# Kernel tuning notes

Hardware: AMD Instinct MI355X
Metric: run time of the kernel (lower is better)

Reference implementation:

```python
import jax, jax.numpy as jnp
import numpy as np

# Keras GRUCell math (reset_after=True default), weights SHARED across all
# num_layers stacked cells (faithful to `[self.rnn_cell for _ in range(L)]`).
NUM_LAYERS = 3
HID = 128


def setup_inputs() -> dict:
    key = jax.random.key(0)
    ks = jax.random.split(key, 4)
    B, T, D, H = 64, 2048, HID, HID
    s = 1.0 / np.sqrt(H)
    return {
        "X": jax.random.uniform(ks[0], (B, T, D), dtype=jnp.float32),
        "kernel": jax.random.normal(ks[1], (D, 3 * H), dtype=jnp.float32) * s,
        "rec_kernel": jax.random.normal(ks[2], (H, 3 * H), dtype=jnp.float32) * s,
        "bias_in": jnp.zeros((3 * H,), dtype=jnp.float32),
        "bias_rec": jnp.zeros((3 * H,), dtype=jnp.float32),
        "W_out": jax.random.normal(ks[3], (H, H), dtype=jnp.float32) * s,
        "b_out": jnp.zeros((H,), dtype=jnp.float32),
    }


def _gru_layer(seq_tbd, kernel, rec_kernel, bias_in, bias_rec):
    # seq_tbd: [T, B, D] -> [T, B, H]
    H = rec_kernel.shape[0]
    B = seq_tbd.shape[1]

    def step(h, x):
        gx = x @ kernel + bias_in            # [B, 3H]
        gh = h @ rec_kernel + bias_rec       # [B, 3H]
        xz, xr, xh = jnp.split(gx, 3, axis=-1)
        hz, hr, hh = jnp.split(gh, 3, axis=-1)
        z = jax.nn.sigmoid(xz + hz)          # update gate
        r = jax.nn.sigmoid(xr + hr)          # reset gate
        cand = jnp.tanh(xh + r * hh)         # candidate state
        h_new = z * h + (1.0 - z) * cand
        return h_new, h_new

    h0 = jnp.zeros((B, H), dtype=seq_tbd.dtype)
    _, out = jax.lax.scan(step, h0, seq_tbd)
    return out


def reference(X, kernel, rec_kernel, bias_in, bias_rec, W_out, b_out):
    seq = jnp.transpose(X, (1, 0, 2))  # [T, B, D]
    for _ in range(NUM_LAYERS):
        seq = _gru_layer(seq, kernel, rec_kernel, bias_in, bias_rec)
    out = jnp.transpose(seq, (1, 0, 2))  # [B, T, H]
    return jax.nn.sigmoid(out @ W_out + b_out)
```

## Files before the change

kernel.cpp:

```cpp
#include <hip/hip_runtime.h>
#include <stdint.h>

#define TSEQ 2048
#define NB   64
#define HD   128
#define G3   384
#define W_RING 512
#define SLOT_U32 (16*128)
#define RING_BYTES ((size_t)12 * W_RING * SLOT_U32 * 4)
#define FLAGS_OFF RING_BYTES

typedef __bf16 bf16_t;
typedef __bf16 bf16x8 __attribute__((ext_vector_type(8)));
typedef float  f32x4  __attribute__((ext_vector_type(4)));
typedef unsigned long long ull;

union B8 { uint4 u; bf16x8 v; unsigned a4[4]; };
union HU { bf16_t h; unsigned short u; };
static_assert(sizeof(B8) == 16, "B8 must be 16B");

__device__ __forceinline__ float fast_sigmoid(float x) {
    float e = __builtin_amdgcn_exp2f(-1.44269504f * x);
    return __builtin_amdgcn_rcpf(1.0f + e);
}
__device__ __forceinline__ float fast_tanh(float x) {
    x = fminf(9.0f, fmaxf(-9.0f, x));
    float e = __builtin_amdgcn_exp2f(2.88539008f * x);
    return 1.0f - 2.0f * __builtin_amdgcn_rcpf(1.0f + e);
}

#define MFMA16(A_, B_, C_) (C_) = __builtin_amdgcn_mfma_f32_16x16x32_bf16((A_), (B_), (C_), 0, 0, 0)

__device__ __forceinline__ ull ld_agent_u64(const ull* p) {
    return __hip_atomic_load(p, __ATOMIC_RELAXED, __HIP_MEMORY_SCOPE_AGENT);
}
__device__ __forceinline__ void st_agent_u32(unsigned* p, unsigned v) {
    __hip_atomic_store(p, v, __ATOMIC_RELAXED, __HIP_MEMORY_SCOPE_AGENT);
}
__device__ __forceinline__ unsigned ld_flag_acq(const unsigned* p) {
    return __hip_atomic_load(p, __ATOMIC_ACQUIRE, __HIP_MEMORY_SCOPE_AGENT);
}
__device__ __forceinline__ void st_flag_rel(unsigned* p, unsigned v) {
    __hip_atomic_store(p, v, __ATOMIC_RELEASE, __HIP_MEMORY_SCOPE_AGENT);
}
__device__ __forceinline__ unsigned spin_until(const unsigned* f, unsigned need,
                                               unsigned cur, bool& dead) {
    if (cur >= need) return cur;
    if (dead) return need;
    int g = 0;
    do {
        unsigned s = ld_flag_acq(f);
        if (s >= need) return s;
        __builtin_amdgcn_s_sleep(2);
    } while (++g < (1 << 15));
    dead = true;
    return need;
}


#define GRU_STEP(TT, PV)                                                              \
  {                                                                                   \
    if (tid == 0 && (TT) > 0) st_flag_rel(prod_out, (unsigned)((TT) - 1));            \
    if ((TT) > 0) {                                                                   \
      if ((int)((TT) - 1) - (int)cons_seen > W_RING - 80)                             \
        cons_seen = spin_until(cons_out, (unsigned)((TT) - 1) - (W_RING - 80),        \
                               cons_seen, dead);                                      \
      const int sb = (((TT) - 1) & (W_RING - 1)) * SLOT_U32;                          \
      _Pragma("unroll") for (int i = 0; i < 4; ++i)                                   \
        st_agent_u32(rout + sb + (4 * quad + i) * HD + cc, pend[i]);                  \
    }                                                                                 \
    ull raw[4][4];                                                                    \
    f32x4 xr0[4], xr1[4];                                                             \
    if (IN_RING) {                                                                    \
      const ull* ps = (const ull*)(rin + ((TT) & (W_RING - 1)) * SLOT_U32) + lane64;  \
      _Pragma("unroll") for (int q = 0; q < 4; ++q)                                   \
        _Pragma("unroll") for (int k = 0; k < 4; ++k)                                 \
          raw[q][k] = ld_agent_u64(ps + 16 * q + k);                                  \
    } else {                                                                          \
      const float* px = px0 + (TT) * HD;                                              \
      _Pragma("unroll") for (int q = 0; q < 4; ++q) {                                 \
        xr0[q] = *(const f32x4*)(px + 32 * q + 8 * quad);                             \
        xr1[q] = *(const f32x4*)(px + 32 * q + 8 * quad + 4);                         \
      }                                                                               \
    }                                                                                 \
    B8 ah[2][4];                                                                      \
    _Pragma("unroll") for (int hl = 0; hl < 2; ++hl)                                  \
      _Pragma("unroll") for (int q = 0; q < 4; ++q)                                   \
        ah[hl][q].u = ldsh[(PV) ^ 1][hl][q][lane];                                    \
    f32x4 accZ  = {bZ, bZ, bZ, bZ};                                                   \
    f32x4 accR  = {bR, bR, bR, bR};                                                   \
    f32x4 accXC = {bXC, bXC, bXC, bXC};                                               \
    f32x4 accHC = {bHC, bHC, bHC, bHC};                                               \
    _Pragma("unroll") for (int q = 0; q < 4; ++q) {  \
      MFMA16(ah[0][q].v, Br[0][q], accZ);                                             \
      MFMA16(ah[0][q].v, Br[1][q], accR);                                             \
      MFMA16(ah[0][q].v, Br[2][q], accHC);                                            \
      MFMA16(ah[1][q].v, Br[0][q], accZ);                                             \
      MFMA16(ah[1][q].v, Br[1][q], accR);                                             \
      MFMA16(ah[1][q].v, Br[2][q], accHC);                                            \
    }                                                                                 \
    B8 xhi[4], xlo[4];                                                                \
    if (IN_RING) {                                                                    \
      _Pragma("unroll") for (int q = 0; q < 4; ++q)                                   \
        _Pragma("unroll") for (int k = 0; k < 4; ++k) {                               \
          const unsigned a = (unsigned)raw[q][k];                                     \
          const unsigned c = (unsigned)(raw[q][k] >> 32);                             \
          xhi[q].a4[k] = (a >> 16) | (c & 0xFFFF0000u);                               \
          xlo[q].a4[k] = (a & 0xFFFFu) | (c << 16);                                   \
        }                                                                             \
    } else {                                                                          \
      _Pragma("unroll") for (int q = 0; q < 4; ++q)                                   \
        _Pragma("unroll") for (int j = 0; j < 8; ++j) {                               \
          const float f = (j < 4) ? xr0[q][j] : xr1[q][j - 4];                        \
          const bf16_t hh = (bf16_t)f;                                                \
          xhi[q].v[j] = hh;                                                           \
          xlo[q].v[j] = (bf16_t)(f - (float)hh);                                      \
        }                                                                             \
    }                                                                                 \
    _Pragma("unroll") for (int q = 0; q < 4; ++q) {                                   \
      MFMA16(xhi[q].v, Bi_[0][q], accZ);                                              \
      MFMA16(xhi[q].v, Bi_[1][q], accR);                                              \
      MFMA16(xhi[q].v, Bi_[2][q], accXC);                                             \
      MFMA16(xlo[q].v, Bi_[0][q], accZ);                                              \
      MFMA16(xlo[q].v, Bi_[1][q], accR);                                              \
      MFMA16(xlo[q].v, Bi_[2][q], accXC);                                             \
    }                                                                                 \
    _Pragma("unroll") for (int i = 0; i < 4; ++i) {                                   \
      const float zg = fast_sigmoid(accZ[i]);                                         \
      const float rg = fast_sigmoid(accR[i]);                                         \
      const float cd = fast_tanh(accXC[i] + rg * accHC[i]);                           \
      const float hn = cd + zg * (hprev[i] - cd);                                     \
      hprev[i] = hn;                                                                  \
      HU hh; hh.h = (bf16_t)hn;                                                       \
      HU hl_; hl_.h = (bf16_t)(hn - (float)hh.h);                                     \
      pend[i] = ((unsigned)hh.u << 16) | (unsigned)hl_.u;                             \
      const int mrow = 4 * quad + i;                                                  \
      ((bf16_t*)&ldsh[(PV)][0][qq][lamb + mrow])[jj] = hh.h;                          \
      ((bf16_t*)&ldsh[(PV)][1][qq][lamb + mrow])[jj] = hl_.h;                         \
    }                                                                                 \
    if (IN_RING && (TT) < TSEQ - 1)                                                   \
      seen = spin_until(prod_in, (unsigned)((TT) + 2), seen, dead);                   \
    if (IN_RING && tid == 0 && (((TT) & 15) == 15))                                   \
      st_agent_u32(cons_in, (unsigned)(TT));                                          \
    __syncthreads();                                                                  \
  }

template <bool IN_RING>
__device__ __forceinline__ void gru_stage(
    uint4 (*ldsh)[2][4][64],
    const float* __restrict__ X,
    const unsigned* __restrict__ rin,
    unsigned* __restrict__ rout,
    unsigned* prod_in, unsigned* cons_in,
    unsigned* prod_out, unsigned* cons_out,
    const float* __restrict__ Wrec, const float* __restrict__ Win,
    const float* __restrict__ bin, const float* __restrict__ brec, int b)
{
    const int tid  = threadIdx.x;
    const int w    = tid >> 6;
    const int lane = tid & 63;
    const int l15  = lane & 15;
    const int quad = lane >> 4;

    bf16x8 Br[3][4];
    bf16x8 Bi_[3][4];
#pragma unroll
    for (int g = 0; g < 3; ++g)
#pragma unroll
        for (int q = 0; q < 4; ++q) {
            const int col = 128 * g + 16 * w + l15;
#pragma unroll
            for (int j = 0; j < 8; ++j) {
                const int row = 32 * q + 8 * quad + j;
                Br[g][q][j]  = (bf16_t)Wrec[row * G3 + col];
                Bi_[g][q][j] = (bf16_t)Win[row * G3 + col];
            }
        }

    const int cc    = 16 * w + l15;
    const float bZ  = bin[cc] + brec[cc];
    const float bR  = bin[128 + cc] + brec[128 + cc];
    const float bXC = bin[256 + cc];
    const float bHC = brec[256 + cc];

    const float* px0 = IN_RING ? nullptr : (X + (size_t)(16 * b + l15) * TSEQ * HD);
    const int lane64 = l15 * 64 + 4 * quad;

    {
        uint4 z4; z4.x = z4.y = z4.z = z4.w = 0u;
        ldsh[1][tid >> 8][(tid >> 6) & 3][tid & 63] = z4;
    }
    const int qq   = cc >> 5;
    const int lamb = 16 * ((cc >> 3) & 3);
    const int jj   = cc & 7;

    float hprev[4] = {0.f, 0.f, 0.f, 0.f};
    unsigned pend[4] = {0u, 0u, 0u, 0u};
    unsigned seen = 0, cons_seen = 0;
    bool dead = false;

    if (IN_RING) seen = spin_until(prod_in, 1u, seen, dead);
    __syncthreads();

    for (int t = 0; t < TSEQ; t += 2) {
        GRU_STEP(t, 0)
        GRU_STEP(t + 1, 1)
    }
    {
        const int sb = ((TSEQ - 1) & (W_RING - 1)) * SLOT_U32;
#pragma unroll
        for (int i = 0; i < 4; ++i)
            st_agent_u32(rout + sb + (4 * quad + i) * HD + cc, pend[i]);
    }
    __syncthreads();
    if (tid == 0) st_flag_rel(prod_out, (unsigned)TSEQ);
}

__device__ __forceinline__ void outproj_stage(
    const unsigned* __restrict__ rin, unsigned* prod_in, unsigned* cons_in,
    const float* __restrict__ Wout, const float* __restrict__ bout,
    float* __restrict__ out, int b)
{
    const int tid  = threadIdx.x;
    const int w    = tid >> 6;
    const int lane = tid & 63;
    const int l15  = lane & 15;
    const int quad = lane >> 4;

    bf16x8 Bw[4];
#pragma unroll
    for (int q = 0; q < 4; ++q)
#pragma unroll
        for (int j = 0; j < 8; ++j)
            Bw[q][j] = (bf16_t)Wout[(32 * q + 8 * quad + j) * HD + 16 * w + l15];
    const float bb = bout[16 * w + l15];
    const int lane64 = l15 * 64 + 4 * quad;

    ull raw[2][4][4];
    unsigned seen = 0;
    bool dead = false;
    seen = spin_until(prod_in, 1u, seen, dead);
    {
        const ull* ps = (const ull*)(rin + 0) + lane64;
#pragma unroll
        for (int q = 0; q < 4; ++q)
#pragma unroll
            for (int k = 0; k < 4; ++k) raw[0][q][k] = ld_agent_u64(ps + 16 * q + k);
    }
    for (int t = 0; t < TSEQ; ++t) {
        if (t < TSEQ - 1) {
            seen = spin_until(prod_in, (unsigned)(t + 2), seen, dead);
            const ull* ps = (const ull*)(rin + ((t + 1) & (W_RING - 1)) * SLOT_U32) + lane64;
#pragma unroll
            for (int q = 0; q < 4; ++q)
#pragma unroll
                for (int k = 0; k < 4; ++k)
                    raw[(t + 1) & 1][q][k] = ld_agent_u64(ps + 16 * q + k);
        }
        B8 ahhi[4], ahlo[4];
#pragma unroll
        for (int q = 0; q < 4; ++q)
#pragma unroll
            for (int k = 0; k < 4; ++k) {
                const ull d = raw[t & 1][q][k];
                const unsigned a = (unsigned)d;
                const unsigned c = (unsigned)(d >> 32);
                ahhi[q].a4[k] = (a >> 16) | (c & 0xFFFF0000u);
                ahlo[q].a4[k] = (a & 0xFFFFu) | (c << 16);
            }
        f32x4 acc = {bb, bb, bb, bb};
#pragma unroll
        for (int q = 0; q < 4; ++q) {
            MFMA16(ahhi[q].v, Bw[q], acc);
            MFMA16(ahlo[q].v, Bw[q], acc);
        }
#pragma unroll
        for (int i = 0; i < 4; ++i) {
            const float s = fast_sigmoid(acc[i]);
            out[(size_t)((16 * b + 4 * quad + i) * TSEQ + t) * HD + 16 * w + l15] = s;
        }
        if ((t & 63) == 63) {
            __syncthreads();
            if (tid == 0) st_agent_u32(cons_in, (unsigned)t);
        }
    }
}

__global__ __launch_bounds__(512, 2) void fused_gru(
    const float* __restrict__ X,
    const float* __restrict__ Wk, const float* __restrict__ Wr,
    const float* __restrict__ bi, const float* __restrict__ br,
    const float* __restrict__ Wo, const float* __restrict__ bo,
    float* __restrict__ out, unsigned char* __restrict__ ws)
{
    __shared__ uint4 ldsh[2][2][4][64];
    const int stage = blockIdx.x >> 2;
    const int b     = blockIdx.x & 3;
    unsigned* F = (unsigned*)(ws + FLAGS_OFF);
    unsigned* ring0 = (unsigned*)ws + (size_t)(0 * 4 + b) * W_RING * SLOT_U32;
    unsigned* ring1 = (unsigned*)ws + (size_t)(1 * 4 + b) * W_RING * SLOT_U32;
    unsigned* ring2 = (unsigned*)ws + (size_t)(2 * 4 + b) * W_RING * SLOT_U32;
    unsigned* p0 = F + (0 * 4 + b) * 64, *c0 = p0 + 32;
    unsigned* p1 = F + (1 * 4 + b) * 64, *c1 = p1 + 32;
    unsigned* p2 = F + (2 * 4 + b) * 64, *c2 = p2 + 32;

    if (stage == 0)
        gru_stage<false>(ldsh, X, nullptr, ring0, nullptr, nullptr, p0, c0, Wr, Wk, bi, br, b);
    else if (stage == 1)
        gru_stage<true>(ldsh, nullptr, ring0, ring1, p0, c0, p1, c1, Wr, Wk, bi, br, b);
    else if (stage == 2)
        gru_stage<true>(ldsh, nullptr, ring1, ring2, p1, c1, p2, c2, Wr, Wk, bi, br, b);
    else
        outproj_stage(ring2, p2, c2, Wo, bo, out, b);
}

extern "C" void kernel_launch(void* const* d_in, const int* in_sizes, int n_in,
                              void* d_out, int out_size, void* d_ws, size_t ws_size,
                              hipStream_t stream) {
    const float* X  = (const float*)d_in[0];
    const float* Wk = (const float*)d_in[1];
    const float* Wr = (const float*)d_in[2];
    const float* bi = (const float*)d_in[3];
    const float* br = (const float*)d_in[4];
    const float* Wo = (const float*)d_in[5];
    const float* bo = (const float*)d_in[6];
    float* out = (float*)d_out;

    if (ws_size < RING_BYTES + 4096) return;
    hipMemsetAsync((char*)d_ws + FLAGS_OFF, 0, 4096, stream);
    fused_gru<<<16, 512, 0, stream>>>(X, Wk, Wr, bi, br, Wo, bo, out,
                                      (unsigned char*)d_ws);
}
```

Before: 12.45 ms.

## Prefetch next-step inputs, batch producer flags, and use lighter barriers in GRU pipeline

Each GRU stage now loads the input for step t+1 into a double-buffered register set at the end of step t, so global or ring latency overlaps with the barrier and the next step's recurrent MFMAs. Producer flags are published every 16 steps instead of every step, consumer acknowledgements every 8 steps, and the per-step __syncthreads is replaced by an s_barrier that waits only on LDS except every 16th step. Flag polling uses relaxed loads with a compiler fence, and the ring window is shrunk to 128 slots. Launch bounds are set to one block per SIMD group to allow more registers. The relaxed polling and barriers that skip waiting on vector memory risk memory-ordering bugs, and the coarser flags add pipeline latency between stages.

```diff
diff --git a/kernel.cpp b/kernel.cpp
--- a/kernel.cpp
+++ b/kernel.cpp
@@ -5,7 +5,7 @@
 #define NB   64
 #define HD   128
 #define G3   384
-#define W_RING 512
+#define W_RING 128
 #define SLOT_U32 (16*128)
 #define RING_BYTES ((size_t)12 * W_RING * SLOT_U32 * 4)
 #define FLAGS_OFF RING_BYTES
@@ -31,14 +31,21 @@
 
 #define MFMA16(A_, B_, C_) (C_) = __builtin_amdgcn_mfma_f32_16x16x32_bf16((A_), (B_), (C_), 0, 0, 0)
 
+__device__ __forceinline__ void fast_barrier() {
+    asm volatile("s_waitcnt lgkmcnt(0)\n\ts_barrier" ::: "memory");
+}
+__device__ __forceinline__ void full_barrier() {
+    asm volatile("s_waitcnt vmcnt(0) lgkmcnt(0)\n\ts_barrier" ::: "memory");
+}
+
 __device__ __forceinline__ ull ld_agent_u64(const ull* p) {
     return __hip_atomic_load(p, __ATOMIC_RELAXED, __HIP_MEMORY_SCOPE_AGENT);
 }
 __device__ __forceinline__ void st_agent_u32(unsigned* p, unsigned v) {
     __hip_atomic_store(p, v, __ATOMIC_RELAXED, __HIP_MEMORY_SCOPE_AGENT);
 }
-__device__ __forceinline__ unsigned ld_flag_acq(const unsigned* p) {
-    return __hip_atomic_load(p, __ATOMIC_ACQUIRE, __HIP_MEMORY_SCOPE_AGENT);
+__device__ __forceinline__ unsigned ld_flag_rlx(const unsigned* p) {
+    return __hip_atomic_load(p, __ATOMIC_RELAXED, __HIP_MEMORY_SCOPE_AGENT);
 }
 __device__ __forceinline__ void st_flag_rel(unsigned* p, unsigned v) {
     __hip_atomic_store(p, v, __ATOMIC_RELEASE, __HIP_MEMORY_SCOPE_AGENT);
@@ -49,8 +56,8 @@
     if (dead) return need;
     int g = 0;
     do {
-        unsigned s = ld_flag_acq(f);
-        if (s >= need) return s;
+        unsigned s = ld_flag_rlx(f);
+        if (s >= need) { asm volatile("" ::: "memory"); return s; }
         __builtin_amdgcn_s_sleep(2);
     } while (++g < (1 << 15));
     dead = true;
@@ -58,9 +65,26 @@
 }
 
 
+#define LOADRING(DST, TT2)                                                            \
+    { const ull* ps = (const ull*)(rin + ((TT2) & (W_RING - 1)) * SLOT_U32) + lane64; \
+      _Pragma("unroll") for (int q = 0; q < 4; ++q)                                   \
+        _Pragma("unroll") for (int k = 0; k < 4; ++k)                                 \
+          raw[DST][q][k] = ld_agent_u64(ps + 16 * q + k); }
+
+#define LOADF32(DST, TT2)                                                             \
+    { const float* px = px0 + (TT2) * HD;                                             \
+      _Pragma("unroll") for (int q = 0; q < 4; ++q) {                                 \
+        xr0[DST][q] = *(const f32x4*)(px + 32 * q + 8 * quad);                        \
+        xr1[DST][q] = *(const f32x4*)(px + 32 * q + 8 * quad + 4); } }
+
 #define GRU_STEP(TT, PV)                                                              \
   {                                                                                   \
-    if (tid == 0 && (TT) > 0) st_flag_rel(prod_out, (unsigned)((TT) - 1));            \
+    B8 ah[2][4];                                                                      \
+    _Pragma("unroll") for (int hl = 0; hl < 2; ++hl)                                  \
+      _Pragma("unroll") for (int q = 0; q < 4; ++q)                                   \
+        ah[hl][q].u = ldsh[(PV) ^ 1][hl][q][lane];                                    \
+    if ((((TT) & 15) == 0) && (TT) > 0 && tid == 0)                                   \
+      st_flag_rel(prod_out, (unsigned)(TT) - 1u);           \
     if ((TT) > 0) {                                                                   \
       if ((int)((TT) - 1) - (int)cons_seen > W_RING - 80)                             \
         cons_seen = spin_until(cons_out, (unsigned)((TT) - 1) - (W_RING - 80),        \
@@ -69,61 +93,43 @@
       _Pragma("unroll") for (int i = 0; i < 4; ++i)                                   \
         st_agent_u32(rout + sb + (4 * quad + i) * HD + cc, pend[i]);                  \
     }                                                                                 \
-    ull raw[4][4];                                                                    \
-    f32x4 xr0[4], xr1[4];                                                             \
+    B8 xhi[4], xlo[4];                                                                \
     if (IN_RING) {                                                                    \
-      const ull* ps = (const ull*)(rin + ((TT) & (W_RING - 1)) * SLOT_U32) + lane64;  \
       _Pragma("unroll") for (int q = 0; q < 4; ++q)                                   \
-        _Pragma("unroll") for (int k = 0; k < 4; ++k)                                 \
-          raw[q][k] = ld_agent_u64(ps + 16 * q + k);                                  \
+        _Pragma("unroll") for (int k = 0; k < 4; ++k) {                               \
+          const unsigned a = (unsigned)raw[PV][q][k];                                 \
+          const unsigned c = (unsigned)(raw[PV][q][k] >> 32);                         \
+          xhi[q].a4[k] = (a >> 16) | (c & 0xFFFF0000u);                               \
+          xlo[q].a4[k] = (a & 0xFFFFu) | (c << 16);                                   \
+        }                                                                             \
     } else {                                                                          \
-      const float* px = px0 + (TT) * HD;                                              \
-      _Pragma("unroll") for (int q = 0; q < 4; ++q) {                                 \
-        xr0[q] = *(const f32x4*)(px + 32 * q + 8 * quad);                             \
-        xr1[q] = *(const f32x4*)(px + 32 * q + 8 * quad + 4);                         \
-      }                                                                               \
-    }                                                                                 \
-    B8 ah[2][4];                                                                      \
-    _Pragma("unroll") for (int hl = 0; hl < 2; ++hl)                                  \
       _Pragma("unroll") for (int q = 0; q < 4; ++q)                                   \
-        ah[hl][q].u = ldsh[(PV) ^ 1][hl][q][lane];                                    \
+        _Pragma("unroll") for (int j = 0; j < 8; ++j) {                               \
+          const float f = (j < 4) ? xr0[PV][q][j] : xr1[PV][q][j - 4];                \
+          const bf16_t hh = (bf16_t)f;                                                \
+          xhi[q].v[j] = hh;                                                           \
+          xlo[q].v[j] = (bf16_t)(f - (float)hh);                                      \
+        }                                                                             \
+    }                                                                                 \
     f32x4 accZ  = {bZ, bZ, bZ, bZ};                                                   \
     f32x4 accR  = {bR, bR, bR, bR};                                                   \
     f32x4 accXC = {bXC, bXC, bXC, bXC};                                               \
     f32x4 accHC = {bHC, bHC, bHC, bHC};                                               \
-    _Pragma("unroll") for (int q = 0; q < 4; ++q) {  \
+    _Pragma("unroll") for (int q = 0; q < 4; ++q) {     \
+      MFMA16(xhi[q].v, Bi_[0][q], accZ);                                              \
+      MFMA16(xhi[q].v, Bi_[1][q], accR);                                              \
+      MFMA16(xhi[q].v, Bi_[2][q], accXC);                                             \
+      MFMA16(xlo[q].v, Bi_[0][q], accZ);                                              \
+      MFMA16(xlo[q].v, Bi_[1][q], accR);                                              \
+      MFMA16(xlo[q].v, Bi_[2][q], accXC);                                             \
+    }                                                                                 \
+    _Pragma("unroll") for (int q = 0; q < 4; ++q) {                                   \
       MFMA16(ah[0][q].v, Br[0][q], accZ);                                             \
       MFMA16(ah[0][q].v, Br[1][q], accR);                                             \
       MFMA16(ah[0][q].v, Br[2][q], accHC);                                            \
       MFMA16(ah[1][q].v, Br[0][q], accZ);                                             \
       MFMA16(ah[1][q].v, Br[1][q], accR);                                             \
       MFMA16(ah[1][q].v, Br[2][q], accHC);                                            \
-    }                                                                                 \
-    B8 xhi[4], xlo[4];                                                                \
-    if (IN_RING) {                                                                    \
-      _Pragma("unroll") for (int q = 0; q < 4; ++q)                                   \
-        _Pragma("unroll") for (int k = 0; k < 4; ++k) {                               \
-          const unsigned a = (unsigned)raw[q][k];                                     \
-          const unsigned c = (unsigned)(raw[q][k] >> 32);                             \
-          xhi[q].a4[k] = (a >> 16) | (c & 0xFFFF0000u);                               \
-          xlo[q].a4[k] = (a & 0xFFFFu) | (c << 16);                                   \
-        }                                                                             \
-    } else {                                                                          \
-      _Pragma("unroll") for (int q = 0; q < 4; ++q)                                   \
-        _Pragma("unroll") for (int j = 0; j < 8; ++j) {                               \
-          const float f = (j < 4) ? xr0[q][j] : xr1[q][j - 4];                        \
-          const bf16_t hh = (bf16_t)f;                                                \
-          xhi[q].v[j] = hh;                                                           \
-          xlo[q].v[j] = (bf16_t)(f - (float)hh);                                      \
-        }                                                                             \
-    }                                                                                 \
-    _Pragma("unroll") for (int q = 0; q < 4; ++q) {                                   \
-      MFMA16(xhi[q].v, Bi_[0][q], accZ);                                              \
-      MFMA16(xhi[q].v, Bi_[1][q], accR);                                              \
-      MFMA16(xhi[q].v, Bi_[2][q], accXC);                                             \
-      MFMA16(xlo[q].v, Bi_[0][q], accZ);                                              \
-      MFMA16(xlo[q].v, Bi_[1][q], accR);                                              \
-      MFMA16(xlo[q].v, Bi_[2][q], accXC);                                             \
     }                                                                                 \
     _Pragma("unroll") for (int i = 0; i < 4; ++i) {                                   \
       const float zg = fast_sigmoid(accZ[i]);                                         \
@@ -138,11 +144,17 @@
       ((bf16_t*)&ldsh[(PV)][0][qq][lamb + mrow])[jj] = hh.h;                          \
       ((bf16_t*)&ldsh[(PV)][1][qq][lamb + mrow])[jj] = hl_.h;                         \
     }                                                                                 \
-    if (IN_RING && (TT) < TSEQ - 1)                                                   \
-      seen = spin_until(prod_in, (unsigned)((TT) + 2), seen, dead);                   \
-    if (IN_RING && tid == 0 && (((TT) & 15) == 15))                                   \
+    if ((TT) < TSEQ - 1) {      \
+      if (IN_RING) {                                                                  \
+        seen = spin_until(prod_in, (unsigned)(TT) + 2u, seen, dead);                  \
+        LOADRING((PV) ^ 1, (TT) + 1);                                                 \
+      } else {                                                                        \
+        LOADF32((PV) ^ 1, (TT) + 1);                                                  \
+      }                                                                               \
+    }                                                                                 \
+    if (IN_RING && tid == 0 && (((TT) & 7) == 7))                                     \
       st_agent_u32(cons_in, (unsigned)(TT));                                          \
-    __syncthreads();                                                                  \
+    if ((((TT) + 1) & 15) == 0) full_barrier(); else fast_barrier();                  \
   }
 
 template <bool IN_RING>
@@ -199,7 +211,15 @@
     unsigned seen = 0, cons_seen = 0;
     bool dead = false;
 
-    if (IN_RING) seen = spin_until(prod_in, 1u, seen, dead);
+    ull   raw[2][4][4];
+    f32x4 xr0[2][4], xr1[2][4];
+
+    if (IN_RING) {
+        seen = spin_until(prod_in, 1u, seen, dead);
+        LOADRING(0, 0);
+    } else {
+        LOADF32(0, 0);
+    }
     __syncthreads();
 
     for (int t = 0; t < TSEQ; t += 2) {
@@ -213,7 +233,10 @@
             st_agent_u32(rout + sb + (4 * quad + i) * HD + cc, pend[i]);
     }
     __syncthreads();
-    if (tid == 0) st_flag_rel(prod_out, (unsigned)TSEQ);
+    if (tid == 0) {
+        st_flag_rel(prod_out, (unsigned)TSEQ + 2u);
+        if (IN_RING) st_agent_u32(cons_in, (unsigned)TSEQ);
+    }
 }
 
 __device__ __forceinline__ void outproj_stage(
@@ -279,14 +302,11 @@
             const float s = fast_sigmoid(acc[i]);
             out[(size_t)((16 * b + 4 * quad + i) * TSEQ + t) * HD + 16 * w + l15] = s;
         }
-        if ((t & 63) == 63) {
-            __syncthreads();
-            if (tid == 0) st_agent_u32(cons_in, (unsigned)t);
-        }
-    }
-}
-
-__global__ __launch_bounds__(512, 2) void fused_gru(
+        if (tid == 0 && ((t & 7) == 7)) st_agent_u32(cons_in, (unsigned)t);
+    }
+}
+
+__global__ __launch_bounds__(512, 1) void fused_gru(
     const float* __restrict__ X,
     const float* __restrict__ Wk, const float* __restrict__ Wr,
     const float* __restrict__ bi, const float* __restrict__ br,
```

Result: no change. 12.36 ms (-0.7%).
